# Optimization experiments

Measured on AMD Instinct MI355X. Metric: run time of the kernel, lower is better.

## Reference

```python
import jax, jax.numpy as jnp
import numpy as np
from jax import lax

B, N_SITES, FEAT, BOND, OUT = 2048, 128, 64, 32, 256
CORE_SCALE = 0.02  # keeps the 128-step matrix product finite


def setup_inputs() -> dict:
    key = jax.random.key(0)
    ks = jax.random.split(key, 6)
    return {
        "x": jax.random.normal(ks[0], (B, N_SITES, FEAT), dtype=jnp.float32),
        "cores": jax.random.normal(ks[1], (N_SITES, BOND, FEAT, BOND), dtype=jnp.float32) * CORE_SCALE,
        "start": jax.random.normal(ks[2], (1, BOND), dtype=jnp.float32),
        "end": jax.random.normal(ks[3], (BOND, 1), dtype=jnp.float32),
        "fc_w": jax.random.normal(ks[4], (OUT, 1), dtype=jnp.float32),
        "fc_b": jax.random.normal(ks[5], (OUT,), dtype=jnp.float32),
    }


def reference(x, cores, start, end, fc_w, fc_b):
    # x: [B, N, F]; cores: [N, D, F, D]; start: [1, D]; end: [D, 1]
    b = x.shape[0]
    res0 = jnp.broadcast_to(start, (b, start.shape[1]))  # [B, D]

    def step(res, site):
        xi, core = site  # xi: [B, F], core: [D, F, D]
        m = jnp.einsum('bf,dfr->bdr', xi, core)  # per-site transfer matrix [B, D, D]
        return jnp.einsum('bd,bdr->br', res, m), None

    res, _ = lax.scan(step, res0, (jnp.swapaxes(x, 0, 1), cores))
    val = res @ end  # [B, 1]
    return val @ fc_w.T + fc_b  # [B, OUT]
```

## Files before the change

### kernel.cpp

```cpp
#include <hip/hip_runtime.h>


#define NSITES 128
#define FEATD  64
#define BOND   32
#define OUTD   256
#define BT     16
#define SEGLEN 32
#define NSEG   (NSITES / SEGLEN)
#define NBT    (2048 / BT)

#define MS_RS  648
#define MS_BS  40

typedef __attribute__((ext_vector_type(4)))  float float4v;
typedef __attribute__((ext_vector_type(16))) float float16v;

__device__ __forceinline__ unsigned pk4_fp8(float a, float b, float c, float d) {
    int v = __builtin_amdgcn_cvt_pk_fp8_f32(a, b, 0, false);
    v = __builtin_amdgcn_cvt_pk_fp8_f32(c, d, v, true);
    return (unsigned)v;
}
__device__ __forceinline__ long mklong(int lo, int hi) {
    return ((long)(unsigned)lo) | (((long)hi) << 32);
}

__global__ __launch_bounds__(256)
void prep_cores8(const float* __restrict__ cores, unsigned char* __restrict__ core8) {
    __shared__ float tile[FEATD][BOND + 4];
    const int nd = blockIdx.x;
    const int t  = threadIdx.x;
    const float* src = cores + (size_t)nd * (FEATD * BOND);
    {
        int base = t * 8;
        int f = base >> 5, r0 = base & 31;
        float4 v0 = *(const float4*)(src + base);
        float4 v1 = *(const float4*)(src + base + 4);
        tile[f][r0 + 0] = v0.x; tile[f][r0 + 1] = v0.y;
        tile[f][r0 + 2] = v0.z; tile[f][r0 + 3] = v0.w;
        tile[f][r0 + 4] = v1.x; tile[f][r0 + 5] = v1.y;
        tile[f][r0 + 6] = v1.z; tile[f][r0 + 7] = v1.w;
    }
    __syncthreads();
    const int r = t >> 3, f0 = (t & 7) * 8;
    const float s = 16.0f;
    unsigned lo = pk4_fp8(tile[f0 + 0][r] * s, tile[f0 + 1][r] * s,
                          tile[f0 + 2][r] * s, tile[f0 + 3][r] * s);
    unsigned hi = pk4_fp8(tile[f0 + 4][r] * s, tile[f0 + 5][r] * s,
                          tile[f0 + 6][r] * s, tile[f0 + 7][r] * s);
    uint2 w; w.x = lo; w.y = hi;
    *(uint2*)(core8 + ((size_t)nd * BOND + r) * FEATD + f0) = w;
}

__device__ __forceinline__ void product_step(const unsigned char* __restrict__ MSb,
                                             int pq[2][4], int wave, int l, int h,
                                             int paddr) {
#pragma unroll
    for (int bi = 0; bi < 2; ++bi) {
        const int bb = wave * 2 + bi;
        long a0 = *(const long*)&MSb[l * MS_RS + bb * MS_BS + 8 * h];
        long a1 = *(const long*)&MSb[l * MS_RS + bb * MS_BS + 16 + 8 * h];
        int x0 = __builtin_amdgcn_ds_bpermute(paddr, pq[bi][0]);
        int x1 = __builtin_amdgcn_ds_bpermute(paddr, pq[bi][1]);
        int x2 = __builtin_amdgcn_ds_bpermute(paddr, pq[bi][2]);
        int x3 = __builtin_amdgcn_ds_bpermute(paddr, pq[bi][3]);
        long bf0 = h ? mklong(x1, pq[bi][1]) : mklong(pq[bi][0], x0);
        long bf1 = h ? mklong(x3, pq[bi][3]) : mklong(pq[bi][2], x2);
        float16v pc;
#pragma unroll
        for (int i = 0; i < 16; ++i) pc[i] = 0.f;
        pc = __builtin_amdgcn_mfma_f32_32x32x16_fp8_fp8(a0, bf0, pc, 0, 0, 0);
        pc = __builtin_amdgcn_mfma_f32_32x32x16_fp8_fp8(a1, bf1, pc, 0, 0, 0);
#pragma unroll
        for (int g = 0; g < 4; ++g)
            pq[bi][g] = (int)pk4_fp8(pc[4 * g + 0] * 0.0625f, pc[4 * g + 1] * 0.0625f,
                                     pc[4 * g + 2] * 0.0625f, pc[4 * g + 3] * 0.0625f);
    }
}

__global__ __launch_bounds__(512, 4)
void mps_seg(const float* __restrict__ x, const unsigned char* __restrict__ core8,
             unsigned char* __restrict__ Pout) {
    __shared__ __align__(16) unsigned char MS[2][BOND * MS_RS];
    __shared__ __align__(16) unsigned char XS[2][BT * 72];

    const int t    = threadIdx.x;
    const int wave = t >> 6;
    const int lane = t & 63;
    const int cl   = lane & 15;
    const int q    = lane >> 4;
    const int l    = lane & 31;
    const int h    = lane >> 5;
    const int b0   = blockIdx.x * BT;
    const int seg  = blockIdx.y;
    const int n0   = seg * SEGLEN;

    int pq[2][4];
    {
        int g0 = l >> 3;
        int hm = ((l >> 2) & 1) == h;
#pragma unroll
        for (int bi = 0; bi < 2; ++bi)
#pragma unroll
            for (int g = 0; g < 4; ++g)
                pq[bi][g] = (g == g0 && hm) ? (0x58 << ((l & 3) * 8)) : 0;
    }
    const int paddr = (lane ^ 32) << 2;

    const int xb = t >> 5, xf = (t & 31) * 2;
    const unsigned afoff = (unsigned)((wave * 128 + cl) * FEATD + q * 8);

    {
        float2 x0 = *(const float2*)(x + ((size_t)(b0 + xb) * NSITES + n0) * FEATD + xf);
        int v = __builtin_amdgcn_cvt_pk_fp8_f32(x0.x, x0.y, 0, false);
        *(unsigned short*)&XS[0][xb * 72 + xf] = (unsigned short)(v & 0xffff);
    }
    float2 xr = *(const float2*)(x + ((size_t)(b0 + xb) * NSITES + n0 + 1) * FEATD + xf);
    long af[16];
    {
        const unsigned char* p0 = core8 + (size_t)n0 * (1024 * FEATD) + afoff;
#pragma unroll
        for (int i = 0; i < 8; ++i) {
            af[i * 2 + 0] = *(const long*)(p0 + i * (16 * FEATD));
            af[i * 2 + 1] = *(const long*)(p0 + i * (16 * FEATD) + 32);
        }
    }
    __syncthreads();

    for (int k = 0; k < SEGLEN; ++k) {
        const int par = k & 1;
        const int n = n0 + k;

        if (k + 1 < SEGLEN) {
            int v = __builtin_amdgcn_cvt_pk_fp8_f32(xr.x, xr.y, 0, false);
            *(unsigned short*)&XS[par ^ 1][xb * 72 + xf] = (unsigned short)(v & 0xffff);
        }
        if (k + 2 < SEGLEN)
            xr = *(const float2*)(x + ((size_t)(b0 + xb) * NSITES + n + 2) * FEATD + xf);

        long bx0 = *(const long*)&XS[par][cl * 72 + q * 8];
        long bx1 = *(const long*)&XS[par][cl * 72 + 32 + q * 8];
#pragma unroll
        for (int p = 0; p < 2; ++p) {
            float4v acc[4];
#pragma unroll
            for (int u = 0; u < 4; ++u) {
                float4v z = {0.f, 0.f, 0.f, 0.f};
                z = __builtin_amdgcn_mfma_f32_16x16x32_fp8_fp8(af[(2 * u + p) * 2], bx0, z, 0, 0, 0);
                acc[u] = __builtin_amdgcn_mfma_f32_16x16x32_fp8_fp8(af[(2 * u + p) * 2 + 1], bx1, z, 0, 0, 0);
            }
#pragma unroll
            for (int g = 0; g < 4; ++g) {
                unsigned w = pk4_fp8(acc[0][g], acc[1][g], acc[2][g], acc[3][g]);
                *(unsigned*)&MS[par][(16 * p + 4 * q + g) * MS_RS + cl * MS_BS + wave * 4] = w;
            }
        }

        if (k + 1 < SEGLEN) {
            const unsigned char* p1 = core8 + (size_t)(n + 1) * (1024 * FEATD) + afoff;
#pragma unroll
            for (int i = 0; i < 8; ++i) {
                af[i * 2 + 0] = *(const long*)(p1 + i * (16 * FEATD));
                af[i * 2 + 1] = *(const long*)(p1 + i * (16 * FEATD) + 32);
            }
        }

        if (k > 0) product_step(MS[par ^ 1], pq, wave, l, h, paddr);

        __syncthreads();
    }
    product_step(MS[(SEGLEN - 1) & 1], pq, wave, l, h, paddr);

#pragma unroll
    for (int bi = 0; bi < 2; ++bi) {
        const int bb = wave * 2 + bi;
        unsigned char* gp = Pout + (((size_t)seg * 2048 + b0 + bb) * 1024);
#pragma unroll
        for (int g = 0; g < 4; ++g)
            *(unsigned*)(gp + l * 32 + 8 * g + 4 * h) = (unsigned)pq[bi][g];
    }
}

__global__ __launch_bounds__(256)
void combine(const unsigned char* __restrict__ Pout, const float* __restrict__ startv,
             const float* __restrict__ endv, const float* __restrict__ fc_w,
             const float* __restrict__ fc_b, float* __restrict__ out) {
    __shared__ __align__(16) unsigned char st[16 * 1024];
    __shared__ float resA[16][34], resB[16][34];
    __shared__ float val_lds[16];
    const int t  = threadIdx.x;
    const int b0 = blockIdx.x * 16;
    const int bt = t >> 4;
    const int c  = t & 15;

    for (int e = t; e < 512; e += 256) resA[e >> 5][e & 31] = startv[e & 31];

    for (int s = 0; s < NSEG; ++s) {
        {
            const uint4* g = (const uint4*)(Pout + ((size_t)s * 2048 + b0) * 1024);
#pragma unroll
            for (int it = 0; it < 4; ++it)
                *(uint4*)&st[(it * 256 + t) * 16] = g[it * 256 + t];
        }
        __syncthreads();
        const float* rin = (s & 1) ? &resB[bt][0] : &resA[bt][0];
        float* rout      = (s & 1) ? &resA[bt][0] : &resB[bt][0];
        float a0 = 0.f, a1 = 0.f;
#pragma unroll
        for (int alpha = 0; alpha < BOND; ++alpha) {
            float rv = rin[alpha];
            unsigned short pp = *(const unsigned short*)&st[bt * 1024 + alpha * 32 + 2 * c];
            a0 += rv * __builtin_amdgcn_cvt_f32_fp8((int)(pp & 0xff), 0);
            a1 += rv * __builtin_amdgcn_cvt_f32_fp8((int)(pp >> 8), 0);
        }
        rout[2 * c]     = a0 * 0.0625f;
        rout[2 * c + 1] = a1 * 0.0625f;
        __syncthreads();
    }

    float pv = resA[bt][2 * c] * endv[2 * c] + resA[bt][2 * c + 1] * endv[2 * c + 1];
#pragma unroll
    for (int off = 1; off < 16; off <<= 1) pv += __shfl_xor(pv, off, 64);
    if (c == 0) val_lds[bt] = pv;
    __syncthreads();

    const float v = val_lds[bt];
#pragma unroll
    for (int i = 0; i < 4; ++i) {
        int j = c * 4 + i * 64;
        float4 w4  = *(const float4*)(fc_w + j);
        float4 bb4 = *(const float4*)(fc_b + j);
        float4 o;
        o.x = v * w4.x + bb4.x;
        o.y = v * w4.y + bb4.y;
        o.z = v * w4.z + bb4.z;
        o.w = v * w4.w + bb4.w;
        *(float4*)(out + (size_t)(b0 + bt) * OUTD + j) = o;
    }
}

extern "C" void kernel_launch(void* const* d_in, const int* in_sizes, int n_in,
                              void* d_out, int out_size, void* d_ws, size_t ws_size,
                              hipStream_t stream) {
    const float* x      = (const float*)d_in[0];
    const float* cores  = (const float*)d_in[1];
    const float* startv = (const float*)d_in[2];
    const float* endv   = (const float*)d_in[3];
    const float* fc_w   = (const float*)d_in[4];
    const float* fc_b   = (const float*)d_in[5];
    float* out = (float*)d_out;

    unsigned char* core8 = (unsigned char*)d_ws;
    unsigned char* Pout  = core8 + (size_t)NSITES * 1024 * FEATD;

    prep_cores8<<<NSITES * BOND, 256, 0, stream>>>(cores, core8);
    mps_seg<<<dim3(NBT, NSEG), 512, 0, stream>>>(x, core8, Pout);
    combine<<<2048 / 16, 256, 0, stream>>>(Pout, startv, endv, fc_w, fc_b, out);
}
```

Before: 245.4 us.

## Halve batch tile to 8 with 256-thread blocks for segment and combine kernels

Shrinks the batch tile per block from 16 to 8 and the block size from 512 to 256 threads. This doubles the grid and cuts shared memory per block, aiming for better CU fill. Each wave now computes all 32 output rows of the transfer matrix, loading the second half of the core fragments inside the loop rather than prefetching it. Half of each 16-wide MFMA's batch columns are now duplicated padding, and total core reads from L2 double. The combine kernel is remapped to one lane per bond index for 8-batch tiles.

Result: slower. 348.6 us (+42.0%).

```diff
diff --git a/kernel.cpp b/kernel.cpp
--- a/kernel.cpp
+++ b/kernel.cpp
@@ -5,12 +5,12 @@
 #define FEATD  64
 #define BOND   32
 #define OUTD   256
-#define BT     16
+#define BT     8
 #define SEGLEN 32
 #define NSEG   (NSITES / SEGLEN)
 #define NBT    (2048 / BT)
 
-#define MS_RS  648
+#define MS_RS  328
 #define MS_BS  40
 
 typedef __attribute__((ext_vector_type(4)))  float float4v;
@@ -71,14 +71,15 @@
         for (int i = 0; i < 16; ++i) pc[i] = 0.f;
         pc = __builtin_amdgcn_mfma_f32_32x32x16_fp8_fp8(a0, bf0, pc, 0, 0, 0);
         pc = __builtin_amdgcn_mfma_f32_32x32x16_fp8_fp8(a1, bf1, pc, 0, 0, 0);
+        pc *= 0.0625f;
 #pragma unroll
         for (int g = 0; g < 4; ++g)
-            pq[bi][g] = (int)pk4_fp8(pc[4 * g + 0] * 0.0625f, pc[4 * g + 1] * 0.0625f,
-                                     pc[4 * g + 2] * 0.0625f, pc[4 * g + 3] * 0.0625f);
-    }
-}
-
-__global__ __launch_bounds__(512, 4)
+            pq[bi][g] = (int)pk4_fp8(pc[4 * g + 0], pc[4 * g + 1],
+                                     pc[4 * g + 2], pc[4 * g + 3]);
+    }
+}
+
+__global__ __launch_bounds__(256, 4)
 void mps_seg(const float* __restrict__ x, const unsigned char* __restrict__ core8,
              unsigned char* __restrict__ Pout) {
     __shared__ __align__(16) unsigned char MS[2][BOND * MS_RS];
@@ -108,7 +109,7 @@
     const int paddr = (lane ^ 32) << 2;
 
     const int xb = t >> 5, xf = (t & 31) * 2;
-    const unsigned afoff = (unsigned)((wave * 128 + cl) * FEATD + q * 8);
+    const int v0 = (wave * 256 + cl) * FEATD + q * 8;
 
     {
         float2 x0 = *(const float2*)(x + ((size_t)(b0 + xb) * NSITES + n0) * FEATD + xf);
@@ -116,13 +117,14 @@
         *(unsigned short*)&XS[0][xb * 72 + xf] = (unsigned short)(v & 0xffff);
     }
     float2 xr = *(const float2*)(x + ((size_t)(b0 + xb) * NSITES + n0 + 1) * FEATD + xf);
-    long af[16];
-    {
-        const unsigned char* p0 = core8 + (size_t)n0 * (1024 * FEATD) + afoff;
-#pragma unroll
-        for (int i = 0; i < 8; ++i) {
-            af[i * 2 + 0] = *(const long*)(p0 + i * (16 * FEATD));
-            af[i * 2 + 1] = *(const long*)(p0 + i * (16 * FEATD) + 32);
+    long af0[16], af1[16];
+    {
+        const unsigned char* cb = core8 + (size_t)n0 * 65536;
+#pragma unroll
+        for (int u = 0; u < 8; ++u) {
+            const unsigned char* pu = cb + u * 2048;
+            af0[2 * u + 0] = *(const long*)(pu + v0);
+            af0[2 * u + 1] = *(const long*)(pu + v0 + 32);
         }
     }
     __syncthreads();
@@ -130,6 +132,7 @@
     for (int k = 0; k < SEGLEN; ++k) {
         const int par = k & 1;
         const int n = n0 + k;
+        const unsigned char* cbn = core8 + (size_t)n * 65536;
 
         if (k + 1 < SEGLEN) {
             int v = __builtin_amdgcn_cvt_pk_fp8_f32(xr.x, xr.y, 0, false);
@@ -138,30 +141,59 @@
         if (k + 2 < SEGLEN)
             xr = *(const float2*)(x + ((size_t)(b0 + xb) * NSITES + n + 2) * FEATD + xf);
 
-        long bx0 = *(const long*)&XS[par][cl * 72 + q * 8];
-        long bx1 = *(const long*)&XS[par][cl * 72 + 32 + q * 8];
-#pragma unroll
-        for (int p = 0; p < 2; ++p) {
-            float4v acc[4];
-#pragma unroll
-            for (int u = 0; u < 4; ++u) {
+#pragma unroll
+        for (int u = 0; u < 8; ++u) {
+            const unsigned char* pu = cbn + u * 2048 + 1024;
+            af1[2 * u + 0] = *(const long*)(pu + v0);
+            af1[2 * u + 1] = *(const long*)(pu + v0 + 32);
+        }
+
+        long bx0 = *(const long*)&XS[par][(cl & 7) * 72 + q * 8];
+        long bx1 = *(const long*)&XS[par][(cl & 7) * 72 + 32 + q * 8];
+        {
+            float4v acc[8];
+#pragma unroll
+            for (int u = 0; u < 8; ++u) {
                 float4v z = {0.f, 0.f, 0.f, 0.f};
-                z = __builtin_amdgcn_mfma_f32_16x16x32_fp8_fp8(af[(2 * u + p) * 2], bx0, z, 0, 0, 0);
-                acc[u] = __builtin_amdgcn_mfma_f32_16x16x32_fp8_fp8(af[(2 * u + p) * 2 + 1], bx1, z, 0, 0, 0);
-            }
-#pragma unroll
-            for (int g = 0; g < 4; ++g) {
-                unsigned w = pk4_fp8(acc[0][g], acc[1][g], acc[2][g], acc[3][g]);
-                *(unsigned*)&MS[par][(16 * p + 4 * q + g) * MS_RS + cl * MS_BS + wave * 4] = w;
+                z = __builtin_amdgcn_mfma_f32_16x16x32_fp8_fp8(af0[2 * u], bx0, z, 0, 0, 0);
+                acc[u] = __builtin_amdgcn_mfma_f32_16x16x32_fp8_fp8(af0[2 * u + 1], bx1, z, 0, 0, 0);
+            }
+            if (cl < 8) {
+#pragma unroll
+                for (int g = 0; g < 4; ++g) {
+                    unsigned d0 = pk4_fp8(acc[0][g], acc[1][g], acc[2][g], acc[3][g]);
+                    unsigned d1 = pk4_fp8(acc[4][g], acc[5][g], acc[6][g], acc[7][g]);
+                    *(long*)&MS[par][(4 * q + g) * MS_RS + cl * MS_BS + wave * 8] =
+                        mklong((int)d0, (int)d1);
+                }
+            }
+        }
+        {
+            float4v acc[8];
+#pragma unroll
+            for (int u = 0; u < 8; ++u) {
+                float4v z = {0.f, 0.f, 0.f, 0.f};
+                z = __builtin_amdgcn_mfma_f32_16x16x32_fp8_fp8(af1[2 * u], bx0, z, 0, 0, 0);
+                acc[u] = __builtin_amdgcn_mfma_f32_16x16x32_fp8_fp8(af1[2 * u + 1], bx1, z, 0, 0, 0);
+            }
+            if (cl < 8) {
+#pragma unroll
+                for (int g = 0; g < 4; ++g) {
+                    unsigned d0 = pk4_fp8(acc[0][g], acc[1][g], acc[2][g], acc[3][g]);
+                    unsigned d1 = pk4_fp8(acc[4][g], acc[5][g], acc[6][g], acc[7][g]);
+                    *(long*)&MS[par][(16 + 4 * q + g) * MS_RS + cl * MS_BS + wave * 8] =
+                        mklong((int)d0, (int)d1);
+                }
             }
         }
 
         if (k + 1 < SEGLEN) {
-            const unsigned char* p1 = core8 + (size_t)(n + 1) * (1024 * FEATD) + afoff;
-#pragma unroll
-            for (int i = 0; i < 8; ++i) {
-                af[i * 2 + 0] = *(const long*)(p1 + i * (16 * FEATD));
-                af[i * 2 + 1] = *(const long*)(p1 + i * (16 * FEATD) + 32);
+            const unsigned char* cb1 = core8 + (size_t)(n + 1) * 65536;
+#pragma unroll
+            for (int u = 0; u < 8; ++u) {
+                const unsigned char* pu = cb1 + u * 2048;
+                af0[2 * u + 0] = *(const long*)(pu + v0);
+                af0[2 * u + 1] = *(const long*)(pu + v0 + 32);
             }
         }
 
@@ -185,49 +217,45 @@
 void combine(const unsigned char* __restrict__ Pout, const float* __restrict__ startv,
              const float* __restrict__ endv, const float* __restrict__ fc_w,
              const float* __restrict__ fc_b, float* __restrict__ out) {
-    __shared__ __align__(16) unsigned char st[16 * 1024];
-    __shared__ float resA[16][34], resB[16][34];
-    __shared__ float val_lds[16];
+    __shared__ __align__(16) unsigned char st[8 * 1024];
+    __shared__ float resA[8][34], resB[8][34];
+    __shared__ float val_lds[8];
     const int t  = threadIdx.x;
-    const int b0 = blockIdx.x * 16;
-    const int bt = t >> 4;
-    const int c  = t & 15;
-
-    for (int e = t; e < 512; e += 256) resA[e >> 5][e & 31] = startv[e & 31];
+    const int b0 = blockIdx.x * 8;
+    const int bt = t >> 5;
+    const int c  = t & 31;
+
+    resA[bt][c] = startv[c];
 
     for (int s = 0; s < NSEG; ++s) {
         {
             const uint4* g = (const uint4*)(Pout + ((size_t)s * 2048 + b0) * 1024);
-#pragma unroll
-            for (int it = 0; it < 4; ++it)
-                *(uint4*)&st[(it * 256 + t) * 16] = g[it * 256 + t];
+            *(uint4*)&st[t * 16]         = g[t];
+            *(uint4*)&st[(256 + t) * 16] = g[256 + t];
         }
         __syncthreads();
         const float* rin = (s & 1) ? &resB[bt][0] : &resA[bt][0];
         float* rout      = (s & 1) ? &resA[bt][0] : &resB[bt][0];
-        float a0 = 0.f, a1 = 0.f;
-#pragma unroll
-        for (int alpha = 0; alpha < BOND; ++alpha) {
-            float rv = rin[alpha];
-            unsigned short pp = *(const unsigned short*)&st[bt * 1024 + alpha * 32 + 2 * c];
-            a0 += rv * __builtin_amdgcn_cvt_f32_fp8((int)(pp & 0xff), 0);
-            a1 += rv * __builtin_amdgcn_cvt_f32_fp8((int)(pp >> 8), 0);
-        }
-        rout[2 * c]     = a0 * 0.0625f;
-        rout[2 * c + 1] = a1 * 0.0625f;
+        float acc = 0.f;
+#pragma unroll
+        for (int alpha = 0; alpha < BOND; ++alpha)
+            acc += rin[alpha] *
+                   __builtin_amdgcn_cvt_f32_fp8((int)st[bt * 1024 + alpha * 32 + c], 0);
+        rout[c] = acc * 0.0625f;
         __syncthreads();
     }
 
-    float pv = resA[bt][2 * c] * endv[2 * c] + resA[bt][2 * c + 1] * endv[2 * c + 1];
-#pragma unroll
-    for (int off = 1; off < 16; off <<= 1) pv += __shfl_xor(pv, off, 64);
+    float pv = resA[bt][c] * endv[c];
+#pragma unroll
+    for (int off = 1; off < 32; off <<= 1) pv += __shfl_xor(pv, off, 32);
     if (c == 0) val_lds[bt] = pv;
     __syncthreads();
 
     const float v = val_lds[bt];
-#pragma unroll
-    for (int i = 0; i < 4; ++i) {
-        int j = c * 4 + i * 64;
+    const int j0 = c * 8;
+#pragma unroll
+    for (int i = 0; i < 2; ++i) {
+        int j = j0 + i * 4;
         float4 w4  = *(const float4*)(fc_w + j);
         float4 bb4 = *(const float4*)(fc_b + j);
         float4 o;
@@ -254,6 +282,6 @@
     unsigned char* Pout  = core8 + (size_t)NSITES * 1024 * FEATD;
 
     prep_cores8<<<NSITES * BOND, 256, 0, stream>>>(cores, core8);
-    mps_seg<<<dim3(NBT, NSEG), 512, 0, stream>>>(x, core8, Pout);
-    combine<<<2048 / 16, 256, 0, stream>>>(Pout, startv, endv, fc_w, fc_b, out);
-}
+    mps_seg<<<dim3(NBT, NSEG), 256, 0, stream>>>(x, core8, Pout);
+    combine<<<2048 / 8, 256, 0, stream>>>(Pout, startv, endv, fc_w, fc_b, out);
+}
```
